# Optimization experiments

Hardware: AMD Instinct MI355X
Metric: run time of the kernel (lower is better)

The kernel has to match this reference:

```python
import jax, jax.numpy as jnp
import numpy as np

IN_CH = 512
NUM_HEADS = 8
DEPTH = IN_CH // NUM_HEADS
IN_FEAT = 37


def setup_inputs() -> dict:
    key = jax.random.key(0)
    ks = jax.random.split(key, 9)
    B, S = 4, 2048
    s_in = 1.0 / np.sqrt(IN_FEAT)
    s_ch = 1.0 / np.sqrt(IN_CH)
    return {
        "x": jax.random.normal(ks[0], (B, S, IN_FEAT), dtype=jnp.float32),
        "Wq": jax.random.uniform(ks[1], (IN_FEAT, IN_CH), jnp.float32, -s_in, s_in),
        "bq": jax.random.uniform(ks[2], (IN_CH,), jnp.float32, -s_in, s_in),
        "Wk": jax.random.uniform(ks[3], (IN_FEAT, IN_CH), jnp.float32, -s_in, s_in),
        "bk": jax.random.uniform(ks[4], (IN_CH,), jnp.float32, -s_in, s_in),
        "Wv": jax.random.uniform(ks[5], (IN_FEAT, IN_CH), jnp.float32, -s_in, s_in),
        "bv": jax.random.uniform(ks[6], (IN_CH,), jnp.float32, -s_in, s_in),
        "Wd": jax.random.uniform(ks[7], (IN_CH, IN_CH), jnp.float32, -s_ch, s_ch),
        "bd": jax.random.uniform(ks[8], (IN_CH,), jnp.float32, -s_ch, s_ch),
    }


def reference(x, Wq, bq, Wk, bk, Wv, bv, Wd, bd):
    B, S, _ = x.shape
    # projections: [B,S,in_ch] -> split into [B,S,H,D]
    q = (x @ Wq + bq).reshape(B, S, NUM_HEADS, DEPTH)
    k = (x @ Wk + bk).reshape(B, S, NUM_HEADS, DEPTH)
    v = (x @ Wv + bv).reshape(B, S, NUM_HEADS, DEPTH)
    scale = 1.0 / jnp.sqrt(jnp.float32(DEPTH))
    # scores: [B,H,Sq,Sk]
    logits = jnp.einsum("bqhd,bkhd->bhqk", q, k) * scale
    attn = jax.nn.softmax(logits, axis=-1)
    out = jnp.einsum("bhqk,bkhd->bqhd", attn, v).reshape(B, S, IN_CH)
    return out @ Wd + bd
```

## Files before the change

### kernel.cpp

```cpp
#include <hip/hip_runtime.h>
#include <hip/hip_bf16.h>
#include <stdint.h>

#define IN_FEAT 37
#define IN_CH 512
#define NUM_HEADS 8
#define DEPTH 64
#define BB 4
#define SS 2048
#define NROWS (BB * SS)

typedef unsigned short u16;
typedef __attribute__((ext_vector_type(4))) unsigned short u16x4;
typedef __attribute__((ext_vector_type(8))) short bf16x8;
typedef __attribute__((ext_vector_type(4))) float f32x4;
typedef __attribute__((ext_vector_type(16))) float f32x16;
typedef __attribute__((ext_vector_type(4))) unsigned u32x4;

#define MFMA16(a, b, c) __builtin_amdgcn_mfma_f32_16x16x32_bf16(a, b, c, 0, 0, 0)
#define MFMA32(a, b, c) __builtin_amdgcn_mfma_f32_32x32x16_bf16(a, b, c, 0, 0, 0)

#define GLDS16(gsrc, ldst)                                                          \
    __builtin_amdgcn_global_load_lds(                                               \
        reinterpret_cast<const __attribute__((address_space(1))) void*>(            \
            reinterpret_cast<uintptr_t>(gsrc)),                                     \
        reinterpret_cast<__attribute__((address_space(3))) void*>(                  \
            reinterpret_cast<uintptr_t>(ldst)),                                     \
        16, 0, 0)

__device__ __forceinline__ u16 f2bf(float f) {
    union { float f; unsigned u; } v;
    v.f = f;
    unsigned r = v.u + 0x7fffu + ((v.u >> 16) & 1u);
    return (u16)(r >> 16);
}

__device__ __forceinline__ unsigned cvt_pk_bf16(float a, float b) {
    unsigned r;
    asm("v_cvt_pk_bf16_f32 %0, %1, %2" : "=v"(r) : "v"(a), "v"(b));
    return r;
}

__device__ __forceinline__ float fexp2(float x) {
    float r;
    asm("v_exp_f32 %0, %1" : "=v"(r) : "v"(x));
    return r;
}

#define XB_ELEMS (NROWS * 64)
#define WT_ELEMS (IN_CH * 64)
#define WD_ELEMS (IN_CH * IN_CH)
#define PACK_TOTAL (XB_ELEMS + 3 * WT_ELEMS + WD_ELEMS)

__global__ __launch_bounds__(256) void pack_all(
    const float* __restrict__ x,
    const float* __restrict__ Wq, const float* __restrict__ Wk,
    const float* __restrict__ Wv, const float* __restrict__ Wd,
    u16* __restrict__ xb, u16* __restrict__ WqT, u16* __restrict__ WkT,
    u16* __restrict__ WvT, u16* __restrict__ WdT)
{
    const float QSC = 0.125f * 1.44269504f;
    int idx = blockIdx.x * 256 + threadIdx.x;
    if (idx < XB_ELEMS) {
        int row = idx >> 6, col = idx & 63;
        xb[idx] = (col < IN_FEAT) ? f2bf(x[row * IN_FEAT + col]) : (u16)0;
    } else if (idx < XB_ELEMS + 3 * WT_ELEMS) {
        int j = idx - XB_ELEMS;
        int mat = j >> 15, rem = j & (WT_ELEMS - 1);
        int c = rem >> 6, i = rem & 63;
        float v = 0.f;
        if (i < IN_FEAT) {
            if (mat == 0)      v = Wq[i * IN_CH + c] * QSC;
            else if (mat == 1) v = Wk[i * IN_CH + c];
            else               v = Wv[i * IN_CH + c];
        }
        (mat == 0 ? WqT : mat == 1 ? WkT : WvT)[rem] = f2bf(v);
    } else if (idx < PACK_TOTAL) {
        int j = idx - (XB_ELEMS + 3 * WT_ELEMS);
        int r = j >> 9, c = j & 511;
        WdT[c * IN_CH + r] = f2bf(Wd[j]);
    }
}

__global__ __launch_bounds__(256) void proj_all(
    const u16* __restrict__ xb, const u16* __restrict__ WqT,
    const u16* __restrict__ WkT, const u16* __restrict__ WvT,
    const float* __restrict__ bqp, const float* __restrict__ bkp,
    const float* __restrict__ bvp,
    u16* __restrict__ qo, u16* __restrict__ ko, u16* __restrict__ vo)
{
    const float QSC = 0.125f * 1.44269504f;
    const int tid = threadIdx.x;
    const int w = tid >> 6, lane = tid & 63;
    const int g = lane >> 4, l15 = lane & 15;
    const f32x4 Z4 = {0.f, 0.f, 0.f, 0.f};

    if (blockIdx.z == 0) {
        const int m0 = blockIdx.y * 64 + w * 16;
        const int n0 = blockIdx.x * 64;

        f32x4 aq[4], ak[4];
#pragma unroll
        for (int nt = 0; nt < 4; ++nt) { aq[nt] = Z4; ak[nt] = Z4; }

#pragma unroll
        for (int k0 = 0; k0 < 64; k0 += 32) {
            bf16x8 wq8 = *(const bf16x8*)&WqT[(m0 + l15) * 64 + k0 + g * 8];
            bf16x8 wk8 = *(const bf16x8*)&WkT[(m0 + l15) * 64 + k0 + g * 8];
#pragma unroll
            for (int nt = 0; nt < 4; ++nt) {
                bf16x8 b8 = *(const bf16x8*)&xb[(n0 + nt * 16 + l15) * 64 + k0 + g * 8];
                aq[nt] = MFMA16(wq8, b8, aq[nt]);
                ak[nt] = MFMA16(wk8, b8, ak[nt]);
            }
        }
        const int c0 = m0 + g * 4;
        const int h = c0 >> 6, d0 = c0 & 63;
        float bq4[4], bk4[4];
#pragma unroll
        for (int r = 0; r < 4; ++r) { bq4[r] = bqp[c0 + r] * QSC; bk4[r] = bkp[c0 + r]; }
#pragma unroll
        for (int nt = 0; nt < 4; ++nt) {
            const int rr = n0 + nt * 16 + l15;
            const int b = rr >> 11, s = rr & 2047;
            const int bh = b * NUM_HEADS + h;
            u16x4 pq, pkk;
#pragma unroll
            for (int r = 0; r < 4; ++r) {
                pq[r]  = f2bf(aq[nt][r] + bq4[r]);
                pkk[r] = f2bf(ak[nt][r] + bk4[r]);
            }
            *(u16x4*)&qo[(bh * SS + s) * DEPTH + d0] = pq;
            *(u16x4*)&ko[bh * (SS * 64) + (s >> 6) * 4096 + (s & 63) * 64 +
                          (d0 ^ ((s & 7) << 3))] = pkk;
        }
    } else {
        const int m0 = blockIdx.x * 64 + w * 16;
        const int n0 = blockIdx.y * 64;

        f32x4 acc[4];
#pragma unroll
        for (int nt = 0; nt < 4; ++nt) acc[nt] = Z4;

#pragma unroll
        for (int k0 = 0; k0 < 64; k0 += 32) {
            bf16x8 a = *(const bf16x8*)&xb[(m0 + l15) * 64 + k0 + g * 8];
#pragma unroll
            for (int nt = 0; nt < 4; ++nt) {
                bf16x8 b8 = *(const bf16x8*)&WvT[(n0 + nt * 16 + l15) * 64 + k0 + g * 8];
                acc[nt] = MFMA16(a, b8, acc[nt]);
            }
        }
        const int s0g = m0 + g * 4;
        const int b = s0g >> 11, ss0 = s0g & 2047;
#pragma unroll
        for (int nt = 0; nt < 4; ++nt) {
            const int n = n0 + nt * 16 + l15;
            const int h = n >> 6, dd = n & 63;
            const int bh = b * NUM_HEADS + h;
            const float bv = bvp[n];
            u16x4 pv;
#pragma unroll
            for (int r = 0; r < 4; ++r) pv[r] = f2bf(acc[nt][r] + bv);
            *(u16x4*)&vo[bh * (SS * 64) + (ss0 >> 6) * 4096 + dd * 64 +
                          ((ss0 & 63) ^ ((dd & 7) << 3))] = pv;
        }
    }
}

#define NT (SS / 64)

__global__ __launch_bounds__(256, 4) void attn_kernel(
    const u16* __restrict__ Qm, const u16* __restrict__ Km,
    const u16* __restrict__ Vm, u16* __restrict__ Om)
{
    __shared__ u16 KL[4][2][2048];
    const int tid = threadIdx.x;
    const int w = tid >> 6, lane = tid & 63;
    const int r31 = lane & 31, lh = lane >> 5;
    const int qgrp = w >> 1, kh = w & 1;

    const int lin = blockIdx.x + gridDim.x * blockIdx.y;
    const int xcd = lin & 7, t7 = lin >> 3;
    const int bx = t7 & 31, bh = xcd + 8 * (t7 >> 5);
    const int qbase = bx * 64 + qgrp * 32;

    const u16* ktg = Km + bh * (SS * 64) + kh * 2048;
    const u16* vtg = Vm + bh * (SS * 64);

    bf16x8 Qf[4];
#pragma unroll
    for (int c = 0; c < 4; ++c)
        Qf[c] = *(const bf16x8*)&Qm[(bh * SS + qbase + r31) * 64 + c * 16 + lh * 8];

    f32x16 O0, O1, Z16;
#pragma unroll
    for (int i = 0; i < 16; ++i) { O0[i] = 0.f; O1[i] = 0.f; Z16[i] = 0.f; }
    float lreg = 0.f;

    auto STAGE_K = [&](int buf, int t) {
        const u16* ks = ktg + t * 4096 + lane * 8;
        u16* kd = &KL[w][buf][0];
#pragma unroll
        for (int i = 0; i < 4; ++i) GLDS16(ks + i * 512, kd + i * 512);
    };

    STAGE_K(0, 0);
    STAGE_K(1, 1);

    for (int t = 0; t < NT; ++t) {
        if (t < NT - 1) asm volatile("s_waitcnt vmcnt(4)" ::: "memory");
        else            asm volatile("s_waitcnt vmcnt(0)" ::: "memory");
        __builtin_amdgcn_sched_barrier(0);

        bf16x8 v[4];
        {
            const u16* vt = vtg + t * 4096;
#pragma unroll
            for (int dt = 0; dt < 2; ++dt)
#pragma unroll
                for (int o = 0; o < 2; ++o) {
                    const int vrow = dt * 32 + r31;
                    v[dt * 2 + o] = *(const bf16x8*)
                        &vt[vrow * 64 + ((kh * 32 + o * 16 + lh * 8) ^ ((vrow & 7) << 3))];
                }
        }

        const u16* kb = &KL[w][t & 1][0];
        bf16x8 kf[4];
#pragma unroll
        for (int c = 0; c < 4; ++c)
            kf[c] = *(const bf16x8*)&kb[r31 * 64 + ((c * 16 + lh * 8) ^ ((r31 & 7) << 3))];

        f32x16 s = MFMA32(kf[0], Qf[0], Z16);
        s = MFMA32(kf[1], Qf[1], s);
        s = MFMA32(kf[2], Qf[2], s);
        s = MFMA32(kf[3], Qf[3], s);

        if (t + 2 < NT) {
            asm volatile("s_waitcnt lgkmcnt(0)" ::: "memory");
            __builtin_amdgcn_sched_barrier(0);
            STAGE_K(t & 1, t + 2);
        }

        unsigned pk[8];
        float ps = 0.f;
#pragma unroll
        for (int j = 0; j < 8; ++j) {
            float a = fexp2(s[2 * j]);
            float b = fexp2(s[2 * j + 1]);
            ps += a + b;
            pk[j] = cvt_pk_bf16(a, b);
        }
        lreg += ps;

        asm("v_permlane32_swap_b32 %0, %1" : "+v"(pk[0]), "+v"(pk[2]));
        asm("v_permlane32_swap_b32 %0, %1" : "+v"(pk[1]), "+v"(pk[3]));
        asm("v_permlane32_swap_b32 %0, %1" : "+v"(pk[4]), "+v"(pk[6]));
        asm("v_permlane32_swap_b32 %0, %1" : "+v"(pk[5]), "+v"(pk[7]));

        union { u32x4 u; bf16x8 b; } f0, f1;
        f0.u = (u32x4){pk[0], pk[1], pk[2], pk[3]};
        f1.u = (u32x4){pk[4], pk[5], pk[6], pk[7]};

        O0 = MFMA32(f0.b, v[0], O0);
        O0 = MFMA32(f1.b, v[1], O0);
        O1 = MFMA32(f0.b, v[2], O1);
        O1 = MFMA32(f1.b, v[3], O1);
    }

    asm volatile("s_waitcnt vmcnt(0)" ::: "memory");
    __syncthreads();
    float lfull = lreg + __shfl_xor(lreg, 32, 64);
    float* sc = (float*)&KL[0][0][0];
    float* scp = sc + qgrp * 2112;
    if (kh == 1) {
#pragma unroll
        for (int i = 0; i < 16; ++i) scp[i * 64 + lane] = O0[i];
#pragma unroll
        for (int i = 0; i < 16; ++i) scp[(16 + i) * 64 + lane] = O1[i];
        scp[2048 + lane] = lfull;
    }
    __syncthreads();
    if (kh == 0) {
#pragma unroll
        for (int i = 0; i < 16; ++i) O0[i] += scp[i * 64 + lane];
#pragma unroll
        for (int i = 0; i < 16; ++i) O1[i] += scp[(16 + i) * 64 + lane];
        const float inv = 1.0f / (lfull + scp[2048 + lane]);
        const int b = bh >> 3, hh = bh & 7;
#pragma unroll
        for (int i = 0; i < 16; ++i) {
            const int qr = (i & 3) + 8 * (i >> 2) + 4 * lh;
            const float invq = __shfl(inv, qr, 64);
            const int srow = qbase + qr;
            u16* orow = &Om[((b * SS + srow) << 9) + hh * 64];
            orow[r31]      = f2bf(O0[i] * invq);
            orow[32 + r31] = f2bf(O1[i] * invq);
        }
    }
}

__global__ __launch_bounds__(256) void out_gemm(
    const u16* __restrict__ A, const u16* __restrict__ BT,
    const float* __restrict__ bd, float* __restrict__ out)
{
    const int tid = threadIdx.x;
    const int w = tid >> 6, lane = tid & 63;
    const int g = lane >> 4, l15 = lane & 15;
    const int m0 = blockIdx.x * 64 + w * 16;
    const int n0 = blockIdx.y * 64;
    const f32x4 Z4 = {0.f, 0.f, 0.f, 0.f};

    f32x4 acc[4];
#pragma unroll
    for (int nt = 0; nt < 4; ++nt) acc[nt] = Z4;

    for (int k0 = 0; k0 < IN_CH; k0 += 32) {
        bf16x8 a = *(const bf16x8*)&A[(m0 + l15) * IN_CH + k0 + g * 8];
#pragma unroll
        for (int nt = 0; nt < 4; ++nt) {
            bf16x8 b = *(const bf16x8*)&BT[(n0 + nt * 16 + l15) * IN_CH + k0 + g * 8];
            acc[nt] = MFMA16(a, b, acc[nt]);
        }
    }
#pragma unroll
    for (int nt = 0; nt < 4; ++nt)
#pragma unroll
        for (int r = 0; r < 4; ++r) {
            const int m = m0 + g * 4 + r;
            const int n = n0 + nt * 16 + l15;
            out[m * IN_CH + n] = acc[nt][r] + bd[n];
        }
}

extern "C" void kernel_launch(void* const* d_in, const int* in_sizes, int n_in,
                              void* d_out, int out_size, void* d_ws, size_t ws_size,
                              hipStream_t stream)
{
    const float* x  = (const float*)d_in[0];
    const float* Wq = (const float*)d_in[1];
    const float* bq = (const float*)d_in[2];
    const float* Wk = (const float*)d_in[3];
    const float* bk = (const float*)d_in[4];
    const float* Wv = (const float*)d_in[5];
    const float* bv = (const float*)d_in[6];
    const float* Wd = (const float*)d_in[7];
    const float* bd = (const float*)d_in[8];
    float* out = (float*)d_out;

    u16* ws  = (u16*)d_ws;
    u16* q   = ws;
    u16* k   = q + NROWS * IN_CH;
    u16* vT  = k + NROWS * IN_CH;
    u16* ao  = vT + NROWS * IN_CH;
    u16* WdT = ao + NROWS * IN_CH;
    u16* xb  = WdT + WD_ELEMS;
    u16* WqT = xb + XB_ELEMS;
    u16* WkT = WqT + WT_ELEMS;
    u16* WvT = WkT + WT_ELEMS;

    pack_all<<<dim3((PACK_TOTAL + 255) / 256), dim3(256), 0, stream>>>(
        x, Wq, Wk, Wv, Wd, xb, WqT, WkT, WvT, WdT);
    proj_all<<<dim3(NROWS / 64, IN_CH / 64, 2), dim3(256), 0, stream>>>(
        xb, WqT, WkT, WvT, bq, bk, bv, q, k, vT);
    attn_kernel<<<dim3(SS / 64, BB * NUM_HEADS), dim3(256), 0, stream>>>(q, k, vT, ao);
    out_gemm<<<dim3(NROWS / 64, IN_CH / 64), dim3(256), 0, stream>>>(ao, WdT, bd, out);
}
```

Measured before the change: 121.1 us.

## Split attention KV sequence four ways per 32-query block instead of two

Each attention block now handles 32 queries with four waves, each covering a quarter of the key/value tiles, instead of two query groups of 32 each split across two waves. The grid doubles to 2048 one-dimensional blocks, and the final reduction sums three partial outputs and row sums through LDS. This is meant to raise parallelism and occupancy. The cost is twice as many Q-tile blocks, each rereading the full K/V stream, so total K/V traffic doubles, and the cross-wave reduction gets larger.

Result: slower. 126.0 us (+4.0%).

```diff
diff --git a/kernel.cpp b/kernel.cpp
--- a/kernel.cpp
+++ b/kernel.cpp
@@ -168,7 +168,7 @@
     }
 }
 
-#define NT (SS / 64)
+#define NT4 (SS / 128)
 
 __global__ __launch_bounds__(256, 4) void attn_kernel(
     const u16* __restrict__ Qm, const u16* __restrict__ Km,
@@ -176,17 +176,17 @@
 {
     __shared__ u16 KL[4][2][2048];
     const int tid = threadIdx.x;
-    const int w = tid >> 6, lane = tid & 63;
+    const int kh = tid >> 6, lane = tid & 63;
     const int r31 = lane & 31, lh = lane >> 5;
-    const int qgrp = w >> 1, kh = w & 1;
-
-    const int lin = blockIdx.x + gridDim.x * blockIdx.y;
+
+    const int lin = blockIdx.x;
     const int xcd = lin & 7, t7 = lin >> 3;
-    const int bx = t7 & 31, bh = xcd + 8 * (t7 >> 5);
-    const int qbase = bx * 64 + qgrp * 32;
-
-    const u16* ktg = Km + bh * (SS * 64) + kh * 2048;
-    const u16* vtg = Vm + bh * (SS * 64);
+    const int bx = t7 & 63, bh = xcd + 8 * (t7 >> 6);
+    const int qbase = bx * 32;
+
+    const u16* ktg = Km + bh * (SS * 64) + (kh >> 1) * 4096 + (kh & 1) * 2048;
+    const u16* vtg = Vm + bh * (SS * 64) + (kh >> 1) * 4096;
+    const int kcol0 = (kh & 1) * 32;
 
     bf16x8 Qf[4];
 #pragma unroll
@@ -198,9 +198,9 @@
     for (int i = 0; i < 16; ++i) { O0[i] = 0.f; O1[i] = 0.f; Z16[i] = 0.f; }
     float lreg = 0.f;
 
-    auto STAGE_K = [&](int buf, int t) {
-        const u16* ks = ktg + t * 4096 + lane * 8;
-        u16* kd = &KL[w][buf][0];
+    auto STAGE_K = [&](int buf, int j) {
+        const u16* ks = ktg + j * 8192 + lane * 8;
+        u16* kd = &KL[kh][buf][0];
 #pragma unroll
         for (int i = 0; i < 4; ++i) GLDS16(ks + i * 512, kd + i * 512);
     };
@@ -208,25 +208,25 @@
     STAGE_K(0, 0);
     STAGE_K(1, 1);
 
-    for (int t = 0; t < NT; ++t) {
-        if (t < NT - 1) asm volatile("s_waitcnt vmcnt(4)" ::: "memory");
-        else            asm volatile("s_waitcnt vmcnt(0)" ::: "memory");
+    for (int j = 0; j < NT4; ++j) {
+        if (j < NT4 - 1) asm volatile("s_waitcnt vmcnt(4)" ::: "memory");
+        else             asm volatile("s_waitcnt vmcnt(0)" ::: "memory");
         __builtin_amdgcn_sched_barrier(0);
 
         bf16x8 v[4];
         {
-            const u16* vt = vtg + t * 4096;
+            const u16* vt = vtg + j * 8192;
 #pragma unroll
             for (int dt = 0; dt < 2; ++dt)
 #pragma unroll
                 for (int o = 0; o < 2; ++o) {
                     const int vrow = dt * 32 + r31;
                     v[dt * 2 + o] = *(const bf16x8*)
-                        &vt[vrow * 64 + ((kh * 32 + o * 16 + lh * 8) ^ ((vrow & 7) << 3))];
+                        &vt[vrow * 64 + ((kcol0 + o * 16 + lh * 8) ^ ((vrow & 7) << 3))];
                 }
         }
 
-        const u16* kb = &KL[w][t & 1][0];
+        const u16* kb = &KL[kh][j & 1][0];
         bf16x8 kf[4];
 #pragma unroll
         for (int c = 0; c < 4; ++c)
@@ -237,20 +237,20 @@
         s = MFMA32(kf[2], Qf[2], s);
         s = MFMA32(kf[3], Qf[3], s);
 
-        if (t + 2 < NT) {
+        if (j + 2 < NT4) {
             asm volatile("s_waitcnt lgkmcnt(0)" ::: "memory");
             __builtin_amdgcn_sched_barrier(0);
-            STAGE_K(t & 1, t + 2);
+            STAGE_K(j & 1, j + 2);
         }
 
         unsigned pk[8];
         float ps = 0.f;
 #pragma unroll
-        for (int j = 0; j < 8; ++j) {
-            float a = fexp2(s[2 * j]);
-            float b = fexp2(s[2 * j + 1]);
+        for (int jj = 0; jj < 8; ++jj) {
+            float a = fexp2(s[2 * jj]);
+            float b = fexp2(s[2 * jj + 1]);
             ps += a + b;
-            pk[j] = cvt_pk_bf16(a, b);
+            pk[jj] = cvt_pk_bf16(a, b);
         }
         lreg += ps;
 
@@ -273,21 +273,27 @@
     __syncthreads();
     float lfull = lreg + __shfl_xor(lreg, 32, 64);
     float* sc = (float*)&KL[0][0][0];
-    float* scp = sc + qgrp * 2112;
-    if (kh == 1) {
-#pragma unroll
-        for (int i = 0; i < 16; ++i) scp[i * 64 + lane] = O0[i];
-#pragma unroll
-        for (int i = 0; i < 16; ++i) scp[(16 + i) * 64 + lane] = O1[i];
-        scp[2048 + lane] = lfull;
+    if (kh != 0) {
+        float* slot = sc + (kh - 1) * 2048;
+#pragma unroll
+        for (int i = 0; i < 16; ++i) slot[i * 64 + lane] = O0[i];
+#pragma unroll
+        for (int i = 0; i < 16; ++i) slot[(16 + i) * 64 + lane] = O1[i];
+        sc[6144 + (kh - 1) * 64 + lane] = lfull;
     }
     __syncthreads();
     if (kh == 0) {
 #pragma unroll
-        for (int i = 0; i < 16; ++i) O0[i] += scp[i * 64 + lane];
-#pragma unroll
-        for (int i = 0; i < 16; ++i) O1[i] += scp[(16 + i) * 64 + lane];
-        const float inv = 1.0f / (lfull + scp[2048 + lane]);
+        for (int p = 0; p < 3; ++p) {
+            float* slot = sc + p * 2048;
+#pragma unroll
+            for (int i = 0; i < 16; ++i) O0[i] += slot[i * 64 + lane];
+#pragma unroll
+            for (int i = 0; i < 16; ++i) O1[i] += slot[(16 + i) * 64 + lane];
+        }
+        const float ltot = lfull + sc[6144 + lane] + sc[6144 + 64 + lane] +
+                           sc[6144 + 128 + lane];
+        const float inv = 1.0f / ltot;
         const int b = bh >> 3, hh = bh & 7;
 #pragma unroll
         for (int i = 0; i < 16; ++i) {
@@ -364,6 +370,6 @@
         x, Wq, Wk, Wv, Wd, xb, WqT, WkT, WvT, WdT);
     proj_all<<<dim3(NROWS / 64, IN_CH / 64, 2), dim3(256), 0, stream>>>(
         xb, WqT, WkT, WvT, bq, bk, bv, q, k, vT);
-    attn_kernel<<<dim3(SS / 64, BB * NUM_HEADS), dim3(256), 0, stream>>>(q, k, vT, ao);
+    attn_kernel<<<dim3((SS / 32) * BB * NUM_HEADS), dim3(256), 0, stream>>>(q, k, vT, ao);
     out_gemm<<<dim3(NROWS / 64, IN_CH / 64), dim3(256), 0, stream>>>(ao, WdT, bd, out);
 }
```
